# Performance work log

Hardware: AMD Instinct MI355X
Metric: run time of the kernel (lower is better)

The kernel has to match this reference:

```python
import jax, jax.numpy as jnp
import numpy as np

B, N, D, H, O = 20000, 32, 128, 256, 128
ATT_SLOPE = 0.01   # nn.LeakyReLU() default inside self.att
ALPHA = 0.2        # leakyrelu slope for attention scores


def _lrelu(v, slope):
    return jnp.where(v > 0, v, slope * v)


def setup_inputs() -> dict:
    key = jax.random.key(0)
    ks = jax.random.split(key, 6)
    x = jax.random.normal(ks[0], (B, D), dtype=jnp.float32)
    neibs = jax.random.normal(ks[1], (B * N, D), dtype=jnp.float32)
    # torch Linear weight is [out,in]; we store transposed [in,out] for x @ W
    W_att = jax.random.normal(ks[2], (D, H), dtype=jnp.float32) / np.sqrt(D)
    W_fcx = jax.random.normal(ks[3], (D, O), dtype=jnp.float32) / np.sqrt(D)
    W_fcn = jax.random.normal(ks[4], (D, O), dtype=jnp.float32) / np.sqrt(D)
    a = jax.random.normal(ks[5], (2 * H, 1), dtype=jnp.float32) * (1.414 * np.sqrt(6.0 / (2 * H + 1)))
    return {"x": x, "neibs": neibs, "W_att": W_att, "W_fcx": W_fcx, "W_fcn": W_fcn, "a": a}


def reference(x, neibs, W_att, W_fcx, W_fcn, a):
    b = x.shape[0]
    n = neibs.shape[0] // b
    # self.att = Linear(no bias) + LeakyReLU(default 0.01)
    x_att = _lrelu(x @ W_att, ATT_SLOPE)                       # [B,H]
    neib_att = _lrelu(neibs @ W_att, ATT_SLOPE).reshape(b, n, -1)  # [B,N,H]
    # cat([x_att.repeat, neib_att]) @ a  ==  x_att @ a[:H] + neib_att @ a[H:]
    h = W_att.shape[1]
    e = _lrelu(x_att @ a[:h, 0] + neib_att @ a[h:, 0][..., None] if False else
               (x_att @ a[:h, 0])[:, None] + jnp.einsum('bnh,h->bn', neib_att, a[h:, 0]), ALPHA)  # [B,N]
    attention = jax.nn.softmax(e, axis=1)                      # softmax over neighbors
    # dropout skipped (eval mode / training=False)
    agg_neib = jnp.einsum('bnd,bn->bd', neibs.reshape(b, n, -1), attention)  # [B,D]
    out = jnp.concatenate([x @ W_fcx, agg_neib @ W_fcn], axis=1)  # combine_fn = cat dim=1
    out = jax.nn.relu(out)                                     # activation
    return out
```

## Files before the change

### kernel.cpp

```cpp
#include <hip/hip_runtime.h>
#include <hip/hip_bf16.h>


#define BB 20000
#define NN 32
#define DD 128
#define HH 256
#define OO 128
#define MB 4
#define ROWS 144
#define AG0 132

typedef __bf16 bf16x8 __attribute__((ext_vector_type(8)));
typedef __bf16 bf16x4 __attribute__((ext_vector_type(4)));
typedef float f32x4 __attribute__((ext_vector_type(4)));

template<int CTRL>
__device__ __forceinline__ float dpp_add(float v) {
    int r = __builtin_amdgcn_update_dpp(0, __builtin_bit_cast(int, v), CTRL, 0xF, 0xF, true);
    return v + __builtin_bit_cast(float, r);
}
__device__ __forceinline__ float red16(float v) {
    v = dpp_add<0x111>(v);
    v = dpp_add<0x112>(v);
    v = dpp_add<0x114>(v);
    v = dpp_add<0x118>(v);
    return v;
}

__global__ void prep_weights(const float* __restrict__ Watt,
                             const float* __restrict__ Wfcx,
                             const float* __restrict__ Wfcn,
                             __bf16* __restrict__ WaT,
                             __bf16* __restrict__ WcT) {
    int idx = blockIdx.x * 256 + threadIdx.x;
    int half = idx >> 15;
    int j = idx & 32767;
    int c = j >> 7, k = j & 127;
    if (half == 0) {
        WaT[j] = (__bf16)Watt[k * HH + c];
    } else {
        float wv = (c < OO) ? Wfcx[k * OO + c] : Wfcn[k * OO + (c - OO)];
        WcT[j] = (__bf16)wv;
    }
}

__launch_bounds__(512, 6)
__global__ void gat_fused(const float* __restrict__ x,
                          const float* __restrict__ neibs,
                          const float* __restrict__ a,
                          const __bf16* __restrict__ WaT,
                          const __bf16* __restrict__ WcT,
                          float* __restrict__ out) {
    __shared__ __bf16 rowsS[ROWS * 128];
    __shared__ __bf16 e_part[8][ROWS];

    const int tid = threadIdx.x;
    const int w   = tid >> 6;
    const int l   = tid & 63;
    const int lr  = l & 15;
    const int lg  = l >> 4;
    const int b0  = blockIdx.x * MB;
    char* rbase = (char*)rowsS;

    const int s = tid >> 5;
    const int stbase = s * 256 + ((8 * (tid & 31)) ^ ((s & 7) << 4));
    int abase[4];
#pragma unroll
    for (int ks = 0; ks < 4; ++ks)
        abase[ks] = lr * 256 + ((ks * 64 + lg * 16) ^ ((lr & 7) << 4));

    float4 nv[8], xv;
    {
        const float4* np4 = (const float4*)(neibs + (size_t)b0 * NN * DD);
#pragma unroll
        for (int it = 0; it < 8; ++it) nv[it] = np4[it * 512 + tid];
        if (tid < 128) xv = ((const float4*)(x + (size_t)b0 * DD))[tid];
    }
    float aX[2], aN[2];
#pragma unroll
    for (int c4 = 0; c4 < 2; ++c4) {
        int col = (w * 2 + c4) * 16 + lr;
        aX[c4] = a[col];
        aN[c4] = a[HH + col];
    }
#pragma unroll
    for (int it = 0; it < 8; ++it) {
        bf16x4 sv = { (__bf16)nv[it].x, (__bf16)nv[it].y, (__bf16)nv[it].z, (__bf16)nv[it].w };
        *(bf16x4*)(rbase + stbase + it * 4096) = sv;
    }
    if (tid < 128) {
        bf16x4 sv = { (__bf16)xv.x, (__bf16)xv.y, (__bf16)xv.z, (__bf16)xv.w };
        *(bf16x4*)(rbase + stbase + 32768) = sv;
    }

    bf16x8 bw[2][4];
#pragma unroll
    for (int c4 = 0; c4 < 2; ++c4)
#pragma unroll
        for (int ks = 0; ks < 4; ++ks)
            bw[c4][ks] = *(const bf16x8*)(WaT + ((w * 2 + c4) * 16 + lr) * 128 + ks * 32 + lg * 8);

    __syncthreads();

#pragma unroll 1
    for (int rt = 0; rt < 8; ++rt) {
        bf16x8 af[4];
#pragma unroll
        for (int ks = 0; ks < 4; ++ks)
            af[ks] = *(const bf16x8*)(rbase + abase[ks] + rt * 4096);
        f32x4 acc[2];
#pragma unroll
        for (int c4 = 0; c4 < 2; ++c4) acc[c4] = (f32x4){0.f, 0.f, 0.f, 0.f};
#pragma unroll
        for (int ks = 0; ks < 4; ++ks)
#pragma unroll
            for (int c4 = 0; c4 < 2; ++c4)
                acc[c4] = __builtin_amdgcn_mfma_f32_16x16x32_bf16(af[ks], bw[c4][ks], acc[c4], 0, 0, 0);
        float ep[4] = {0.f, 0.f, 0.f, 0.f};
#pragma unroll
        for (int c4 = 0; c4 < 2; ++c4)
#pragma unroll
            for (int i = 0; i < 4; ++i) {
                float v = acc[c4][i];
                float lv = fmaxf(v, 0.f) + 0.01f * fminf(v, 0.f);
                ep[i] = fmaf(lv, aN[c4], ep[i]);
            }
#pragma unroll
        for (int i = 0; i < 4; ++i) ep[i] = red16(ep[i]);
        if (lr == 15) {
            bf16x4 st = { (__bf16)ep[0], (__bf16)ep[1], (__bf16)ep[2], (__bf16)ep[3] };
            *(bf16x4*)((char*)e_part + w * (2 * ROWS) + rt * 32 + lg * 8) = st;
        }
    }
    {
        bf16x8 af[4];
#pragma unroll
        for (int ks = 0; ks < 4; ++ks)
            af[ks] = *(const bf16x8*)(rbase + abase[ks] + 32768);
        f32x4 acc[2];
#pragma unroll
        for (int c4 = 0; c4 < 2; ++c4) acc[c4] = (f32x4){0.f, 0.f, 0.f, 0.f};
#pragma unroll
        for (int ks = 0; ks < 4; ++ks)
#pragma unroll
            for (int c4 = 0; c4 < 2; ++c4)
                acc[c4] = __builtin_amdgcn_mfma_f32_16x16x32_bf16(af[ks], bw[c4][ks], acc[c4], 0, 0, 0);
        float ep[4] = {0.f, 0.f, 0.f, 0.f};
#pragma unroll
        for (int c4 = 0; c4 < 2; ++c4)
#pragma unroll
            for (int i = 0; i < 4; ++i) {
                float v = acc[c4][i];
                float lv = fmaxf(v, 0.f) + 0.01f * fminf(v, 0.f);
                ep[i] = fmaf(lv, aX[c4], ep[i]);
            }
#pragma unroll
        for (int i = 0; i < 4; ++i) ep[i] = red16(ep[i]);
        if (lr == 15) {
            bf16x4 st = { (__bf16)ep[0], (__bf16)ep[1], (__bf16)ep[2], (__bf16)ep[3] };
            *(bf16x4*)((char*)e_part + w * (2 * ROWS) + 256 + lg * 8) = st;
        }
    }
    __syncthreads();

    const int node = w & 3;
    float att;
    {
        const int nl = l & 31;
        const int idx = node * 32 + nl;
        const int xr = 128 + node;
        float e = 0.f;
#pragma unroll
        for (int wv = 0; wv < 8; ++wv)
            e += (float)e_part[wv][idx] + (float)e_part[wv][xr];
        e = (e > 0.f) ? e : 0.2f * e;
        float mx = e;
#pragma unroll
        for (int m = 16; m >= 1; m >>= 1) mx = fmaxf(mx, __shfl_xor(mx, m, 32));
        float ex = __expf(e - mx);
        float sum = ex;
#pragma unroll
        for (int m = 16; m >= 1; m >>= 1) sum += __shfl_xor(sum, m, 32);
        att = ex / sum;
    }

    bf16x8 bff[2][4];
#pragma unroll
    for (int c4 = 0; c4 < 2; ++c4)
#pragma unroll
        for (int ks = 0; ks < 4; ++ks)
            bff[c4][ks] = *(const bf16x8*)(WcT + ((w * 2 + c4) * 16 + lr) * 128 + ks * 32 + lg * 8);

    {
        const int d = ((w >> 2) << 6) + l;
        const int agb = node * 8192 + 2 * d;
        float ag = 0.f;
#pragma unroll
        for (int n = 0; n < 32; ++n) {
            float wv = __shfl(att, n);
            __bf16 v = *(const __bf16*)(rbase + (((agb + n * 256)) ^ ((n & 7) << 4)));
            ag = fmaf(wv, (float)v, ag);
        }
        int row = AG0 + node;
        int off = row * 256 + ((2 * d) ^ ((row & 7) << 4));
        *(__bf16*)(rbase + off) = (__bf16)ag;
    }
    __syncthreads();

    {
        bf16x8 af[4];
#pragma unroll
        for (int ks = 0; ks < 4; ++ks)
            af[ks] = *(const bf16x8*)(rbase + abase[ks] + 32768);
        f32x4 acc[2];
#pragma unroll
        for (int c4 = 0; c4 < 2; ++c4) acc[c4] = (f32x4){0.f, 0.f, 0.f, 0.f};
#pragma unroll
        for (int ks = 0; ks < 4; ++ks)
#pragma unroll
            for (int c4 = 0; c4 < 2; ++c4)
                acc[c4] = __builtin_amdgcn_mfma_f32_16x16x32_bf16(af[ks], bff[c4][ks], acc[c4], 0, 0, 0);
#pragma unroll
        for (int c4 = 0; c4 < 2; ++c4) {
            int col = (w * 2 + c4) * 16 + lr;
#pragma unroll
            for (int reg = 0; reg < 4; ++reg) {
                int i = lg * 4 + reg;
                bool doit = (col < 128) ? (i < 4) : (i >= 4 && i < 8);
                if (doit) {
                    float v = fmaxf(acc[c4][reg], 0.f);
                    out[(size_t)(b0 + (i & 3)) * 256 + col] = v;
                }
            }
        }
    }
}

extern "C" void kernel_launch(void* const* d_in, const int* in_sizes, int n_in,
                              void* d_out, int out_size, void* d_ws, size_t ws_size,
                              hipStream_t stream) {
    const float* x    = (const float*)d_in[0];
    const float* nb   = (const float*)d_in[1];
    const float* Watt = (const float*)d_in[2];
    const float* Wfcx = (const float*)d_in[3];
    const float* Wfcn = (const float*)d_in[4];
    const float* a    = (const float*)d_in[5];
    __bf16* WaT = (__bf16*)d_ws;
    __bf16* WcT = WaT + 128 * 256;
    float* o = (float*)d_out;

    prep_weights<<<256, 256, 0, stream>>>(Watt, Wfcx, Wfcn, WaT, WcT);
    gat_fused<<<BB / MB, 512, 0, stream>>>(x, nb, a, WaT, WcT, o);
}
```

Baseline: 132.1 us.

## Process two node groups per block, prefetching the second group's neighbors during the first

Each block now handles two groups of 4 nodes, so the grid is halved. The second group's neighbor and x rows are loaded into registers while the first group runs its score, softmax, aggregation and output stages. This hides global-load latency behind MFMA and LDS work. It also merges the neighbor and self score passes into one 9-iteration loop and lowers the launch-bounds occupancy target from 6 to 4, which costs resident waves in exchange for more registers.

```diff
diff --git a/kernel.cpp b/kernel.cpp
--- a/kernel.cpp
+++ b/kernel.cpp
@@ -9,7 +9,7 @@
 #define OO 128
 #define MB 4
 #define ROWS 144
-#define AG0 132
+#define GRID 2500
 
 typedef __bf16 bf16x8 __attribute__((ext_vector_type(8)));
 typedef __bf16 bf16x4 __attribute__((ext_vector_type(4)));
@@ -45,7 +45,7 @@
     }
 }
 
-__launch_bounds__(512, 6)
+__launch_bounds__(512, 4)
 __global__ void gat_fused(const float* __restrict__ x,
                           const float* __restrict__ neibs,
                           const float* __restrict__ a,
@@ -60,22 +60,16 @@
     const int l   = tid & 63;
     const int lr  = l & 15;
     const int lg  = l >> 4;
-    const int b0  = blockIdx.x * MB;
     char* rbase = (char*)rowsS;
 
     const int s = tid >> 5;
     const int stbase = s * 256 + ((8 * (tid & 31)) ^ ((s & 7) << 4));
-    int abase[4];
-#pragma unroll
-    for (int ks = 0; ks < 4; ++ks)
+    const int lrc = lr & 7;
+    int abase[4], fbase[4];
+#pragma unroll
+    for (int ks = 0; ks < 4; ++ks) {
         abase[ks] = lr * 256 + ((ks * 64 + lg * 16) ^ ((lr & 7) << 4));
-
-    float4 nv[8], xv;
-    {
-        const float4* np4 = (const float4*)(neibs + (size_t)b0 * NN * DD);
-#pragma unroll
-        for (int it = 0; it < 8; ++it) nv[it] = np4[it * 512 + tid];
-        if (tid < 128) xv = ((const float4*)(x + (size_t)b0 * DD))[tid];
+        fbase[ks] = lrc * 256 + ((ks * 64 + lg * 16) ^ (lrc << 4));
     }
     float aX[2], aN[2];
 #pragma unroll
@@ -84,14 +78,28 @@
         aX[c4] = a[col];
         aN[c4] = a[HH + col];
     }
-#pragma unroll
-    for (int it = 0; it < 8; ++it) {
-        bf16x4 sv = { (__bf16)nv[it].x, (__bf16)nv[it].y, (__bf16)nv[it].z, (__bf16)nv[it].w };
-        *(bf16x4*)(rbase + stbase + it * 4096) = sv;
-    }
-    if (tid < 128) {
-        bf16x4 sv = { (__bf16)xv.x, (__bf16)xv.y, (__bf16)xv.z, (__bf16)xv.w };
-        *(bf16x4*)(rbase + stbase + 32768) = sv;
+    const int node = w & 3;
+    const int nl = l & 31;
+
+    const int g0 = (int)blockIdx.x * 2;
+    const float4* np4 = (const float4*)neibs + (size_t)g0 * 4096;
+    const float4* xp4 = (const float4*)x + (size_t)g0 * 128;
+
+    {
+        float4 nv[8];
+#pragma unroll
+        for (int it = 0; it < 8; ++it) nv[it] = np4[it * 512 + tid];
+        float4 xv;
+        if (tid < 128) xv = xp4[tid];
+#pragma unroll
+        for (int it = 0; it < 8; ++it) {
+            bf16x4 sv = { (__bf16)nv[it].x, (__bf16)nv[it].y, (__bf16)nv[it].z, (__bf16)nv[it].w };
+            *(bf16x4*)(rbase + stbase + it * 4096) = sv;
+        }
+        if (tid < 128) {
+            bf16x4 sv = { (__bf16)xv.x, (__bf16)xv.y, (__bf16)xv.z, (__bf16)xv.w };
+            *(bf16x4*)(rbase + stbase + 32768) = sv;
+        }
     }
 
     bf16x8 bw[2][4];
@@ -101,75 +109,49 @@
         for (int ks = 0; ks < 4; ++ks)
             bw[c4][ks] = *(const bf16x8*)(WaT + ((w * 2 + c4) * 16 + lr) * 128 + ks * 32 + lg * 8);
 
-    __syncthreads();
-
-#pragma unroll 1
-    for (int rt = 0; rt < 8; ++rt) {
-        bf16x8 af[4];
-#pragma unroll
-        for (int ks = 0; ks < 4; ++ks)
-            af[ks] = *(const bf16x8*)(rbase + abase[ks] + rt * 4096);
-        f32x4 acc[2];
-#pragma unroll
-        for (int c4 = 0; c4 < 2; ++c4) acc[c4] = (f32x4){0.f, 0.f, 0.f, 0.f};
-#pragma unroll
-        for (int ks = 0; ks < 4; ++ks)
-#pragma unroll
-            for (int c4 = 0; c4 < 2; ++c4)
-                acc[c4] = __builtin_amdgcn_mfma_f32_16x16x32_bf16(af[ks], bw[c4][ks], acc[c4], 0, 0, 0);
-        float ep[4] = {0.f, 0.f, 0.f, 0.f};
-#pragma unroll
-        for (int c4 = 0; c4 < 2; ++c4)
-#pragma unroll
-            for (int i = 0; i < 4; ++i) {
-                float v = acc[c4][i];
-                float lv = fmaxf(v, 0.f) + 0.01f * fminf(v, 0.f);
-                ep[i] = fmaf(lv, aN[c4], ep[i]);
+    float4 nv1[8], xv1;
+#pragma unroll
+    for (int it = 0; it < 8; ++it) nv1[it] = np4[4096 + it * 512 + tid];
+    if (tid < 128) xv1 = xp4[128 + tid];
+
+    auto SCORE = [&]() {
+#pragma unroll 2
+        for (int rt = 0; rt < 9; ++rt) {
+            const int off = (rt < 8) ? rt * 4096 : 32768;
+            bf16x8 af[4];
+#pragma unroll
+            for (int ks = 0; ks < 4; ++ks)
+                af[ks] = *(const bf16x8*)(rbase + abase[ks] + off);
+            f32x4 acc[2];
+            acc[0] = (f32x4){0.f, 0.f, 0.f, 0.f};
+            acc[1] = (f32x4){0.f, 0.f, 0.f, 0.f};
+#pragma unroll
+            for (int ks = 0; ks < 4; ++ks)
+#pragma unroll
+                for (int c4 = 0; c4 < 2; ++c4)
+                    acc[c4] = __builtin_amdgcn_mfma_f32_16x16x32_bf16(af[ks], bw[c4][ks], acc[c4], 0, 0, 0);
+            float ep[4] = {0.f, 0.f, 0.f, 0.f};
+#pragma unroll
+            for (int c4 = 0; c4 < 2; ++c4) {
+                float av = (rt == 8) ? aX[c4] : aN[c4];
+#pragma unroll
+                for (int i = 0; i < 4; ++i) {
+                    float v = acc[c4][i];
+                    float lv = fmaxf(v, 0.f) + 0.01f * fminf(v, 0.f);
+                    ep[i] = fmaf(lv, av, ep[i]);
+                }
             }
 #pragma unroll
-        for (int i = 0; i < 4; ++i) ep[i] = red16(ep[i]);
-        if (lr == 15) {
-            bf16x4 st = { (__bf16)ep[0], (__bf16)ep[1], (__bf16)ep[2], (__bf16)ep[3] };
-            *(bf16x4*)((char*)e_part + w * (2 * ROWS) + rt * 32 + lg * 8) = st;
-        }
-    }
-    {
-        bf16x8 af[4];
-#pragma unroll
-        for (int ks = 0; ks < 4; ++ks)
-            af[ks] = *(const bf16x8*)(rbase + abase[ks] + 32768);
-        f32x4 acc[2];
-#pragma unroll
-        for (int c4 = 0; c4 < 2; ++c4) acc[c4] = (f32x4){0.f, 0.f, 0.f, 0.f};
-#pragma unroll
-        for (int ks = 0; ks < 4; ++ks)
-#pragma unroll
-            for (int c4 = 0; c4 < 2; ++c4)
-                acc[c4] = __builtin_amdgcn_mfma_f32_16x16x32_bf16(af[ks], bw[c4][ks], acc[c4], 0, 0, 0);
-        float ep[4] = {0.f, 0.f, 0.f, 0.f};
-#pragma unroll
-        for (int c4 = 0; c4 < 2; ++c4)
-#pragma unroll
-            for (int i = 0; i < 4; ++i) {
-                float v = acc[c4][i];
-                float lv = fmaxf(v, 0.f) + 0.01f * fminf(v, 0.f);
-                ep[i] = fmaf(lv, aX[c4], ep[i]);
+            for (int i = 0; i < 4; ++i) ep[i] = red16(ep[i]);
+            if (lr == 15) {
+                bf16x4 st = { (__bf16)ep[0], (__bf16)ep[1], (__bf16)ep[2], (__bf16)ep[3] };
+                *(bf16x4*)((char*)e_part + w * (2 * ROWS) + rt * 32 + lg * 8) = st;
             }
-#pragma unroll
-        for (int i = 0; i < 4; ++i) ep[i] = red16(ep[i]);
-        if (lr == 15) {
-            bf16x4 st = { (__bf16)ep[0], (__bf16)ep[1], (__bf16)ep[2], (__bf16)ep[3] };
-            *(bf16x4*)((char*)e_part + w * (2 * ROWS) + 256 + lg * 8) = st;
-        }
-    }
-    __syncthreads();
-
-    const int node = w & 3;
-    float att;
-    {
-        const int nl = l & 31;
+        }
+    };
+
+    auto SOFTMAX = [&](int xr) -> float {
         const int idx = node * 32 + nl;
-        const int xr = 128 + node;
         float e = 0.f;
 #pragma unroll
         for (int wv = 0; wv < 8; ++wv)
@@ -182,45 +164,36 @@
         float sum = ex;
 #pragma unroll
         for (int m = 16; m >= 1; m >>= 1) sum += __shfl_xor(sum, m, 32);
-        att = ex / sum;
-    }
-
-    bf16x8 bff[2][4];
-#pragma unroll
-    for (int c4 = 0; c4 < 2; ++c4)
-#pragma unroll
-        for (int ks = 0; ks < 4; ++ks)
-            bff[c4][ks] = *(const bf16x8*)(WcT + ((w * 2 + c4) * 16 + lr) * 128 + ks * 32 + lg * 8);
-
-    {
+        return ex / sum;
+    };
+
+    auto AGG = [&](float att, int aggrow) {
         const int d = ((w >> 2) << 6) + l;
         const int agb = node * 8192 + 2 * d;
         float ag = 0.f;
 #pragma unroll
         for (int n = 0; n < 32; ++n) {
             float wv = __shfl(att, n);
-            __bf16 v = *(const __bf16*)(rbase + (((agb + n * 256)) ^ ((n & 7) << 4)));
+            __bf16 v = *(const __bf16*)(rbase + ((agb + n * 256) ^ ((n & 7) << 4)));
             ag = fmaf(wv, (float)v, ag);
         }
-        int row = AG0 + node;
-        int off = row * 256 + ((2 * d) ^ ((row & 7) << 4));
+        int off = aggrow * 256 + ((2 * d) ^ ((aggrow & 7) << 4));
         *(__bf16*)(rbase + off) = (__bf16)ag;
-    }
-    __syncthreads();
-
-    {
+    };
+
+    auto FINAL = [&](int slotoff, int b0, bf16x8 (&bf)[2][4]) {
         bf16x8 af[4];
 #pragma unroll
         for (int ks = 0; ks < 4; ++ks)
-            af[ks] = *(const bf16x8*)(rbase + abase[ks] + 32768);
+            af[ks] = *(const bf16x8*)(rbase + fbase[ks] + slotoff);
         f32x4 acc[2];
-#pragma unroll
-        for (int c4 = 0; c4 < 2; ++c4) acc[c4] = (f32x4){0.f, 0.f, 0.f, 0.f};
+        acc[0] = (f32x4){0.f, 0.f, 0.f, 0.f};
+        acc[1] = (f32x4){0.f, 0.f, 0.f, 0.f};
 #pragma unroll
         for (int ks = 0; ks < 4; ++ks)
 #pragma unroll
             for (int c4 = 0; c4 < 2; ++c4)
-                acc[c4] = __builtin_amdgcn_mfma_f32_16x16x32_bf16(af[ks], bff[c4][ks], acc[c4], 0, 0, 0);
+                acc[c4] = __builtin_amdgcn_mfma_f32_16x16x32_bf16(af[ks], bf[c4][ks], acc[c4], 0, 0, 0);
 #pragma unroll
         for (int c4 = 0; c4 < 2; ++c4) {
             int col = (w * 2 + c4) * 16 + lr;
@@ -228,13 +201,45 @@
             for (int reg = 0; reg < 4; ++reg) {
                 int i = lg * 4 + reg;
                 bool doit = (col < 128) ? (i < 4) : (i >= 4 && i < 8);
-                if (doit) {
-                    float v = fmaxf(acc[c4][reg], 0.f);
-                    out[(size_t)(b0 + (i & 3)) * 256 + col] = v;
-                }
+                if (doit) out[(size_t)(b0 + (i & 3)) * 256 + col] = fmaxf(acc[c4][reg], 0.f);
             }
         }
-    }
+    };
+
+    __syncthreads();
+    SCORE();
+    __syncthreads();
+    float att0 = SOFTMAX(128 + node);
+    bf16x8 bff[2][4];
+#pragma unroll
+    for (int c4 = 0; c4 < 2; ++c4)
+#pragma unroll
+        for (int ks = 0; ks < 4; ++ks)
+            bff[c4][ks] = *(const bf16x8*)(WcT + ((w * 2 + c4) * 16 + lr) * 128 + ks * 32 + lg * 8);
+    AGG(att0, 132 + node);
+    __syncthreads();
+    FINAL(32768, g0 * MB, bff);
+#pragma unroll
+    for (int it = 0; it < 8; ++it) {
+        bf16x4 sv = { (__bf16)nv1[it].x, (__bf16)nv1[it].y, (__bf16)nv1[it].z, (__bf16)nv1[it].w };
+        *(bf16x4*)(rbase + stbase + it * 4096) = sv;
+    }
+    if (tid < 128) {
+        bf16x4 sv = { (__bf16)xv1.x, (__bf16)xv1.y, (__bf16)xv1.z, (__bf16)xv1.w };
+        *(bf16x4*)(rbase + stbase + 34816) = sv;
+    }
+#pragma unroll
+    for (int c4 = 0; c4 < 2; ++c4)
+#pragma unroll
+        for (int ks = 0; ks < 4; ++ks)
+            bw[c4][ks] = *(const bf16x8*)(WaT + ((w * 2 + c4) * 16 + lr) * 128 + ks * 32 + lg * 8);
+    __syncthreads();
+    SCORE();
+    __syncthreads();
+    float att1 = SOFTMAX(136 + node);
+    AGG(att1, 140 + node);
+    __syncthreads();
+    FINAL(34816, g0 * MB + MB, bff);
 }
 
 extern "C" void kernel_launch(void* const* d_in, const int* in_sizes, int n_in,
@@ -251,5 +256,5 @@
     float* o = (float*)d_out;
 
     prep_weights<<<256, 256, 0, stream>>>(Watt, Wfcx, Wfcn, WaT, WcT);
-    gat_fused<<<BB / MB, 512, 0, stream>>>(x, nb, a, WaT, WcT, o);
-}
+    gat_fused<<<GRID, 512, 0, stream>>>(x, nb, a, WaT, WcT, o);
+}
```

Result: slower. 157.9 us (+19.5%).

## Split x-path into separate kernel and software-pipeline neighbor tiles in persistent blocks

Applied to the files above, without the earlier changes.

Moves the x-dependent work (x@W_fcx output and the x attention score) into a separate prep_x kernel that batches 32 nodes per block and writes e_x to workspace. The main kernel now runs 1000 blocks, each looping over 20 nodes in groups of 4, and prefetches the next neighbor tile into registers while computing the current one. The aggregation is reorganized to use vectorized LDS reads with cross-lane reductions, and only the W_fcn half of the final GEMM remains. Together these aim to hide global load latency and cut wasted MFMA work, at the cost of an extra kernel launch, a workspace round trip for e_x, and higher register pressure.

```diff
diff --git a/kernel.cpp b/kernel.cpp
--- a/kernel.cpp
+++ b/kernel.cpp
@@ -7,13 +7,13 @@
 #define DD 128
 #define HH 256
 #define OO 128
-#define MB 4
-#define ROWS 144
-#define AG0 132
 
 typedef __bf16 bf16x8 __attribute__((ext_vector_type(8)));
 typedef __bf16 bf16x4 __attribute__((ext_vector_type(4)));
 typedef float f32x4 __attribute__((ext_vector_type(4)));
+
+#define LBAR() do { asm volatile("s_waitcnt lgkmcnt(0)" ::: "memory"); \
+                    __builtin_amdgcn_s_barrier(); } while (0)
 
 template<int CTRL>
 __device__ __forceinline__ float dpp_add(float v) {
@@ -45,193 +45,259 @@
     }
 }
 
-__launch_bounds__(512, 6)
-__global__ void gat_fused(const float* __restrict__ x,
-                          const float* __restrict__ neibs,
-                          const float* __restrict__ a,
-                          const __bf16* __restrict__ WaT,
-                          const __bf16* __restrict__ WcT,
-                          float* __restrict__ out) {
-    __shared__ __bf16 rowsS[ROWS * 128];
-    __shared__ __bf16 e_part[8][ROWS];
-
+__launch_bounds__(256, 4)
+__global__ void prep_x(const float* __restrict__ x,
+                       const float* __restrict__ a,
+                       const __bf16* __restrict__ WaT,
+                       const __bf16* __restrict__ WcT,
+                       float* __restrict__ out,
+                       float* __restrict__ e_x) {
+    __shared__ __bf16 xs[32 * 128];
+    __shared__ float esc[4][32];
     const int tid = threadIdx.x;
-    const int w   = tid >> 6;
-    const int l   = tid & 63;
-    const int lr  = l & 15;
-    const int lg  = l >> 4;
-    const int b0  = blockIdx.x * MB;
-    char* rbase = (char*)rowsS;
-
-    const int s = tid >> 5;
-    const int stbase = s * 256 + ((8 * (tid & 31)) ^ ((s & 7) << 4));
+    const int w = tid >> 6, l = tid & 63, lr = l & 15, lg = l >> 4;
+    const int r0 = blockIdx.x * 32;
+    char* xb = (char*)xs;
+
+    {
+        int row = tid >> 3, fb = (tid & 7) * 4;
+        const float4* xp4 = (const float4*)x + (size_t)r0 * 32;
+        float4 v0 = xp4[row * 32 + fb + 0], v1 = xp4[row * 32 + fb + 1];
+        float4 v2 = xp4[row * 32 + fb + 2], v3 = xp4[row * 32 + fb + 3];
+        bf16x8 s0 = { (__bf16)v0.x,(__bf16)v0.y,(__bf16)v0.z,(__bf16)v0.w,
+                      (__bf16)v1.x,(__bf16)v1.y,(__bf16)v1.z,(__bf16)v1.w };
+        bf16x8 s1 = { (__bf16)v2.x,(__bf16)v2.y,(__bf16)v2.z,(__bf16)v2.w,
+                      (__bf16)v3.x,(__bf16)v3.y,(__bf16)v3.z,(__bf16)v3.w };
+        *(bf16x8*)(xb + ((row * 256 + fb * 8)      ^ ((row & 7) << 4))) = s0;
+        *(bf16x8*)(xb + ((row * 256 + fb * 8 + 16) ^ ((row & 7) << 4))) = s1;
+    }
+    __syncthreads();
+
     int abase[4];
 #pragma unroll
     for (int ks = 0; ks < 4; ++ks)
         abase[ks] = lr * 256 + ((ks * 64 + lg * 16) ^ ((lr & 7) << 4));
-
-    float4 nv[8], xv;
-    {
-        const float4* np4 = (const float4*)(neibs + (size_t)b0 * NN * DD);
-#pragma unroll
-        for (int it = 0; it < 8; ++it) nv[it] = np4[it * 512 + tid];
-        if (tid < 128) xv = ((const float4*)(x + (size_t)b0 * DD))[tid];
-    }
-    float aX[2], aN[2];
+    bf16x8 af[2][4];
+#pragma unroll
+    for (int rt = 0; rt < 2; ++rt)
+#pragma unroll
+        for (int ks = 0; ks < 4; ++ks)
+            af[rt][ks] = *(const bf16x8*)(xb + abase[ks] + rt * 4096);
+
+    float ep[2][4] = {{0.f,0.f,0.f,0.f},{0.f,0.f,0.f,0.f}};
+#pragma unroll
+    for (int cc = 0; cc < 6; ++cc) {
+        const int ct = w + 4 * cc;
+        const int col = ct * 16 + lr;
+        const __bf16* bs = (ct < 8) ? (WcT + (size_t)col * 128)
+                                    : (WaT + (size_t)(col - 128) * 128);
+        bf16x8 bw[4];
+#pragma unroll
+        for (int ks = 0; ks < 4; ++ks)
+            bw[ks] = *(const bf16x8*)(bs + ks * 32 + lg * 8);
+#pragma unroll
+        for (int rt = 0; rt < 2; ++rt) {
+            f32x4 acc = (f32x4){0.f, 0.f, 0.f, 0.f};
+#pragma unroll
+            for (int ks = 0; ks < 4; ++ks)
+                acc = __builtin_amdgcn_mfma_f32_16x16x32_bf16(af[rt][ks], bw[ks], acc, 0, 0, 0);
+            if (ct < 8) {
+#pragma unroll
+                for (int i = 0; i < 4; ++i)
+                    out[(size_t)(r0 + rt * 16 + 4 * lg + i) * 256 + col] = fmaxf(acc[i], 0.f);
+            } else {
+                float av = a[col - 128];
+#pragma unroll
+                for (int i = 0; i < 4; ++i) {
+                    float vv = acc[i];
+                    float lv = fmaxf(vv, 0.f) + 0.01f * fminf(vv, 0.f);
+                    ep[rt][i] = fmaf(lv, av, ep[rt][i]);
+                }
+            }
+        }
+    }
+#pragma unroll
+    for (int rt = 0; rt < 2; ++rt)
+#pragma unroll
+        for (int i = 0; i < 4; ++i) ep[rt][i] = red16(ep[rt][i]);
+    if (lr == 15)
+#pragma unroll
+        for (int rt = 0; rt < 2; ++rt)
+#pragma unroll
+            for (int i = 0; i < 4; ++i)
+                esc[w][rt * 16 + 4 * lg + i] = ep[rt][i];
+    __syncthreads();
+    if (tid < 32)
+        e_x[r0 + tid] = esc[0][tid] + esc[1][tid] + esc[2][tid] + esc[3][tid];
+}
+
+__launch_bounds__(512, 4)
+__global__ void gat_main(const float* __restrict__ neibs,
+                         const float* __restrict__ a,
+                         const __bf16* __restrict__ WaT,
+                         const __bf16* __restrict__ WcT,
+                         const float* __restrict__ e_x,
+                         float* __restrict__ out) {
+    __shared__ __bf16 rowsS[128 * 128];
+    __shared__ __bf16 aggA[16 * 128];
+    __shared__ __bf16 e2[128][8];
+
+    const int tid = threadIdx.x;
+    const int w  = tid >> 6;
+    const int l  = tid & 63;
+    const int lr = l & 15;
+    const int lg = l >> 4;
+    const int q  = w & 3;
+    const int dh = w >> 2;
+    char* rb = (char*)rowsS;
+    char* ab = (char*)aggA;
+
+    int abase[4];
+#pragma unroll
+    for (int ks = 0; ks < 4; ++ks)
+        abase[ks] = lr * 256 + ((ks * 64 + lg * 16) ^ ((lr & 7) << 4));
+
+    const int srow = 32 * q + (l >> 1);
+    const int scol = dh * 128 + (l & 1) * 64;
+    const size_t sg4 = (size_t)srow * 32 + dh * 16 + (l & 1) * 8;
+
+    bf16x8 bw[2][4];
+    float aN[2];
 #pragma unroll
     for (int c4 = 0; c4 < 2; ++c4) {
         int col = (w * 2 + c4) * 16 + lr;
-        aX[c4] = a[col];
+#pragma unroll
+        for (int ks = 0; ks < 4; ++ks)
+            bw[c4][ks] = *(const bf16x8*)(WaT + (size_t)col * 128 + ks * 32 + lg * 8);
         aN[c4] = a[HH + col];
     }
-#pragma unroll
-    for (int it = 0; it < 8; ++it) {
-        bf16x4 sv = { (__bf16)nv[it].x, (__bf16)nv[it].y, (__bf16)nv[it].z, (__bf16)nv[it].w };
-        *(bf16x4*)(rbase + stbase + it * 4096) = sv;
-    }
-    if (tid < 128) {
-        bf16x4 sv = { (__bf16)xv.x, (__bf16)xv.y, (__bf16)xv.z, (__bf16)xv.w };
-        *(bf16x4*)(rbase + stbase + 32768) = sv;
-    }
-
-    bf16x8 bw[2][4];
-#pragma unroll
-    for (int c4 = 0; c4 < 2; ++c4)
+    bf16x8 bff[4];
+    {
+        int colf = 128 + w * 16 + lr;
 #pragma unroll
         for (int ks = 0; ks < 4; ++ks)
-            bw[c4][ks] = *(const bf16x8*)(WaT + ((w * 2 + c4) * 16 + lr) * 128 + ks * 32 + lg * 8);
-
+            bff[ks] = *(const bf16x8*)(WcT + (size_t)colf * 128 + ks * 32 + lg * 8);
+    }
+
+    const float4* np4 = (const float4*)neibs;
+    float4 pf[8];
+    auto STAGE_WRITE = [&]() {
+#pragma unroll
+        for (int k = 0; k < 4; ++k) {
+            float4 u = pf[2 * k], v = pf[2 * k + 1];
+            bf16x8 s = { (__bf16)u.x,(__bf16)u.y,(__bf16)u.z,(__bf16)u.w,
+                         (__bf16)v.x,(__bf16)v.y,(__bf16)v.z,(__bf16)v.w };
+            *(bf16x8*)(rb + ((srow * 256 + scol + k * 16) ^ ((srow & 7) << 4))) = s;
+        }
+    };
+
+    int g0 = (int)blockIdx.x * 20;
+
+    {
+        size_t tb = (size_t)g0 * 1024 + sg4;
+#pragma unroll
+        for (int i = 0; i < 8; ++i) pf[i] = np4[tb + i];
+        STAGE_WRITE();
+    }
     __syncthreads();
 
 #pragma unroll 1
-    for (int rt = 0; rt < 8; ++rt) {
-        bf16x8 af[4];
-#pragma unroll
-        for (int ks = 0; ks < 4; ++ks)
-            af[ks] = *(const bf16x8*)(rbase + abase[ks] + rt * 4096);
-        f32x4 acc[2];
-#pragma unroll
-        for (int c4 = 0; c4 < 2; ++c4) acc[c4] = (f32x4){0.f, 0.f, 0.f, 0.f};
-#pragma unroll
-        for (int ks = 0; ks < 4; ++ks)
+    for (int t = 0; t < 5; ++t, g0 += 4) {
+        float exv = e_x[g0 + q];
+        if (t < 4) {
+            size_t tb = (size_t)(g0 + 4) * 1024 + sg4;
+#pragma unroll
+            for (int i = 0; i < 8; ++i) pf[i] = np4[tb + i];
+        }
+
+#pragma unroll
+        for (int rt = 0; rt < 8; ++rt) {
+            bf16x8 af[4];
+#pragma unroll
+            for (int ks = 0; ks < 4; ++ks)
+                af[ks] = *(const bf16x8*)(rb + abase[ks] + rt * 4096);
+            f32x4 acc[2];
+            acc[0] = (f32x4){0.f,0.f,0.f,0.f};
+            acc[1] = (f32x4){0.f,0.f,0.f,0.f};
+#pragma unroll
+            for (int ks = 0; ks < 4; ++ks)
+#pragma unroll
+                for (int c4 = 0; c4 < 2; ++c4)
+                    acc[c4] = __builtin_amdgcn_mfma_f32_16x16x32_bf16(af[ks], bw[c4][ks], acc[c4], 0, 0, 0);
+            float ep[4] = {0.f, 0.f, 0.f, 0.f};
 #pragma unroll
             for (int c4 = 0; c4 < 2; ++c4)
-                acc[c4] = __builtin_amdgcn_mfma_f32_16x16x32_bf16(af[ks], bw[c4][ks], acc[c4], 0, 0, 0);
-        float ep[4] = {0.f, 0.f, 0.f, 0.f};
-#pragma unroll
-        for (int c4 = 0; c4 < 2; ++c4)
-#pragma unroll
-            for (int i = 0; i < 4; ++i) {
-                float v = acc[c4][i];
-                float lv = fmaxf(v, 0.f) + 0.01f * fminf(v, 0.f);
-                ep[i] = fmaf(lv, aN[c4], ep[i]);
-            }
-#pragma unroll
-        for (int i = 0; i < 4; ++i) ep[i] = red16(ep[i]);
-        if (lr == 15) {
-            bf16x4 st = { (__bf16)ep[0], (__bf16)ep[1], (__bf16)ep[2], (__bf16)ep[3] };
-            *(bf16x4*)((char*)e_part + w * (2 * ROWS) + rt * 32 + lg * 8) = st;
-        }
-    }
-    {
-        bf16x8 af[4];
-#pragma unroll
-        for (int ks = 0; ks < 4; ++ks)
-            af[ks] = *(const bf16x8*)(rbase + abase[ks] + 32768);
-        f32x4 acc[2];
-#pragma unroll
-        for (int c4 = 0; c4 < 2; ++c4) acc[c4] = (f32x4){0.f, 0.f, 0.f, 0.f};
-#pragma unroll
-        for (int ks = 0; ks < 4; ++ks)
-#pragma unroll
-            for (int c4 = 0; c4 < 2; ++c4)
-                acc[c4] = __builtin_amdgcn_mfma_f32_16x16x32_bf16(af[ks], bw[c4][ks], acc[c4], 0, 0, 0);
-        float ep[4] = {0.f, 0.f, 0.f, 0.f};
-#pragma unroll
-        for (int c4 = 0; c4 < 2; ++c4)
-#pragma unroll
-            for (int i = 0; i < 4; ++i) {
-                float v = acc[c4][i];
-                float lv = fmaxf(v, 0.f) + 0.01f * fminf(v, 0.f);
-                ep[i] = fmaf(lv, aX[c4], ep[i]);
-            }
-#pragma unroll
-        for (int i = 0; i < 4; ++i) ep[i] = red16(ep[i]);
-        if (lr == 15) {
-            bf16x4 st = { (__bf16)ep[0], (__bf16)ep[1], (__bf16)ep[2], (__bf16)ep[3] };
-            *(bf16x4*)((char*)e_part + w * (2 * ROWS) + 256 + lg * 8) = st;
-        }
-    }
-    __syncthreads();
-
-    const int node = w & 3;
-    float att;
-    {
-        const int nl = l & 31;
-        const int idx = node * 32 + nl;
-        const int xr = 128 + node;
-        float e = 0.f;
-#pragma unroll
-        for (int wv = 0; wv < 8; ++wv)
-            e += (float)e_part[wv][idx] + (float)e_part[wv][xr];
-        e = (e > 0.f) ? e : 0.2f * e;
-        float mx = e;
-#pragma unroll
-        for (int m = 16; m >= 1; m >>= 1) mx = fmaxf(mx, __shfl_xor(mx, m, 32));
-        float ex = __expf(e - mx);
-        float sum = ex;
-#pragma unroll
-        for (int m = 16; m >= 1; m >>= 1) sum += __shfl_xor(sum, m, 32);
-        att = ex / sum;
-    }
-
-    bf16x8 bff[2][4];
-#pragma unroll
-    for (int c4 = 0; c4 < 2; ++c4)
-#pragma unroll
-        for (int ks = 0; ks < 4; ++ks)
-            bff[c4][ks] = *(const bf16x8*)(WcT + ((w * 2 + c4) * 16 + lr) * 128 + ks * 32 + lg * 8);
-
-    {
-        const int d = ((w >> 2) << 6) + l;
-        const int agb = node * 8192 + 2 * d;
-        float ag = 0.f;
-#pragma unroll
-        for (int n = 0; n < 32; ++n) {
+#pragma unroll
+                for (int i = 0; i < 4; ++i) {
+                    float v = acc[c4][i];
+                    float lv = fmaxf(v, 0.f) + 0.01f * fminf(v, 0.f);
+                    ep[i] = fmaf(lv, aN[c4], ep[i]);
+                }
+#pragma unroll
+            for (int i = 0; i < 4; ++i) ep[i] = red16(ep[i]);
+            if (lr == 15)
+#pragma unroll
+                for (int i = 0; i < 4; ++i)
+                    e2[rt * 16 + 4 * lg + i][w] = (__bf16)ep[i];
+        }
+        LBAR();
+
+        float att;
+        {
+            const int nl = l & 31;
+            bf16x8 ev = *(const bf16x8*)(&e2[q * 32 + nl][0]);
+            float e = exv;
+#pragma unroll
+            for (int j = 0; j < 8; ++j) e += (float)ev[j];
+            e = (e > 0.f) ? e : 0.2f * e;
+            float mx = e;
+#pragma unroll
+            for (int m = 16; m >= 1; m >>= 1) mx = fmaxf(mx, __shfl_xor(mx, m, 32));
+            float ex = __expf(e - mx);
+            float sum = ex;
+#pragma unroll
+            for (int m = 16; m >= 1; m >>= 1) sum += __shfl_xor(sum, m, 32);
+            att = ex / sum;
+        }
+
+        const int dq = l & 15, ngrp = l >> 4;
+        float ag[4] = {0.f, 0.f, 0.f, 0.f};
+#pragma unroll
+        for (int j = 0; j < 8; ++j) {
+            int n = ngrp + 4 * j;
             float wv = __shfl(att, n);
-            __bf16 v = *(const __bf16*)(rbase + (((agb + n * 256)) ^ ((n & 7) << 4)));
-            ag = fmaf(wv, (float)v, ag);
-        }
-        int row = AG0 + node;
-        int off = row * 256 + ((2 * d) ^ ((row & 7) << 4));
-        *(__bf16*)(rbase + off) = (__bf16)ag;
-    }
-    __syncthreads();
-
-    {
-        bf16x8 af[4];
-#pragma unroll
-        for (int ks = 0; ks < 4; ++ks)
-            af[ks] = *(const bf16x8*)(rbase + abase[ks] + 32768);
-        f32x4 acc[2];
-#pragma unroll
-        for (int c4 = 0; c4 < 2; ++c4) acc[c4] = (f32x4){0.f, 0.f, 0.f, 0.f};
-#pragma unroll
-        for (int ks = 0; ks < 4; ++ks)
-#pragma unroll
-            for (int c4 = 0; c4 < 2; ++c4)
-                acc[c4] = __builtin_amdgcn_mfma_f32_16x16x32_bf16(af[ks], bff[c4][ks], acc[c4], 0, 0, 0);
-#pragma unroll
-        for (int c4 = 0; c4 < 2; ++c4) {
-            int col = (w * 2 + c4) * 16 + lr;
-#pragma unroll
-            for (int reg = 0; reg < 4; ++reg) {
-                int i = lg * 4 + reg;
-                bool doit = (col < 128) ? (i < 4) : (i >= 4 && i < 8);
-                if (doit) {
-                    float v = fmaxf(acc[c4][reg], 0.f);
-                    out[(size_t)(b0 + (i & 3)) * 256 + col] = v;
-                }
+            int row = 32 * q + n;
+            bf16x4 vv = *(const bf16x4*)(rb + ((row * 256 + dh * 128 + dq * 8) ^ ((row & 7) << 4)));
+#pragma unroll
+            for (int c = 0; c < 4; ++c) ag[c] = fmaf(wv, (float)vv[c], ag[c]);
+        }
+#pragma unroll
+        for (int c = 0; c < 4; ++c) {
+            ag[c] += __shfl_xor(ag[c], 16);
+            ag[c] += __shfl_xor(ag[c], 32);
+        }
+
+        if (t < 4) STAGE_WRITE();
+
+        if (ngrp == 0) {
+            bf16x4 s = { (__bf16)ag[0], (__bf16)ag[1], (__bf16)ag[2], (__bf16)ag[3] };
+            *(bf16x4*)(ab + ((q * 256 + dh * 128 + dq * 8) ^ ((q & 7) << 4))) = s;
+        }
+        LBAR();
+
+        {
+            bf16x8 aff[4];
+#pragma unroll
+            for (int ks = 0; ks < 4; ++ks)
+                aff[ks] = *(const bf16x8*)(ab + abase[ks]);
+            f32x4 accf = (f32x4){0.f, 0.f, 0.f, 0.f};
+#pragma unroll
+            for (int ks = 0; ks < 4; ++ks)
+                accf = __builtin_amdgcn_mfma_f32_16x16x32_bf16(aff[ks], bff[ks], accf, 0, 0, 0);
+            if (lg == 0) {
+#pragma unroll
+                for (int reg = 0; reg < 4; ++reg)
+                    out[(size_t)(g0 + reg) * 256 + 128 + w * 16 + lr] = fmaxf(accf[reg], 0.f);
             }
         }
     }
@@ -247,9 +313,11 @@
     const float* Wfcn = (const float*)d_in[4];
     const float* a    = (const float*)d_in[5];
     __bf16* WaT = (__bf16*)d_ws;
-    __bf16* WcT = WaT + 128 * 256;
-    float* o = (float*)d_out;
+    __bf16* WcT = WaT + 32768;
+    float*  e_x = (float*)(WcT + 32768);
+    float*  o   = (float*)d_out;
 
     prep_weights<<<256, 256, 0, stream>>>(Watt, Wfcx, Wfcn, WaT, WcT);
-    gat_fused<<<BB / MB, 512, 0, stream>>>(x, nb, a, WaT, WcT, o);
-}
+    prep_x<<<625, 256, 0, stream>>>(x, a, WaT, WcT, o, e_x);
+    gat_main<<<1000, 512, 0, stream>>>(nb, a, WaT, WcT, e_x, o);
+}
```

Measured after the change: 156.0 us. 18.1% more time.
